# Kernel optimization log

Hardware: AMD Instinct MI355X
Metric: run time of the kernel (lower is better)

The kernel has to match this reference:

```python
import jax, jax.numpy as jnp
import numpy as np

N, CIN, T, V = 16, 16, 512, 200
K, COUT, H = 3, 64, 64


def setup_inputs() -> dict:
    key = jax.random.key(0)
    ks = jax.random.split(key, 9)
    s = 0.05
    return {
        "x": jax.random.normal(ks[0], (N, CIN, T, V), jnp.float32),
        "A": jax.random.uniform(ks[1], (K, V, V), jnp.float32) / V,
        "W_gcn": jax.random.normal(ks[2], (K * COUT, CIN), jnp.float32) * s,
        "b_gcn": jnp.zeros((K * COUT,), jnp.float32),
        "W_ih": jax.random.normal(ks[3], (4 * H, COUT), jnp.float32) * s,
        "W_hh": jax.random.normal(ks[4], (4 * H, H), jnp.float32) * s,
        "b_ih": jnp.zeros((4 * H,), jnp.float32),
        "b_hh": jnp.zeros((4 * H,), jnp.float32),
        "W_fc": jax.random.normal(ks[5], (1, H), jnp.float32) * s,
        "b_fc": jnp.zeros((1,), jnp.float32),
    }


def reference(x, A, W_gcn, b_gcn, W_ih, W_hh, b_ih, b_hh, W_fc, b_fc):
    n, c, t, v = x.shape
    k = A.shape[0]
    cout = W_gcn.shape[0] // k
    # ConvTemporalGraphical: 1x1 conv -> (n, k*cout, t, v), reshape, adjacency einsum
    y = jnp.einsum('nctv,oc->notv', x, W_gcn) + b_gcn[None, :, None, None]
    y = y.reshape(n, k, cout, t, v)
    y = jnp.einsum('nkctv,kvw->nctw', y, A)  # (n, cout, t, v)
    # mean over node dim, residual=False -> res=0
    y = jnp.mean(y, axis=3)  # (n, cout, t)
    seq = jnp.transpose(y, (2, 0, 1))  # (t, n, cout) time-major for scan

    def step(carry, xt):
        h, ccell = carry
        gates = xt @ W_ih.T + b_ih + h @ W_hh.T + b_hh  # (n, 4H)
        i, f, g, o = jnp.split(gates, 4, axis=-1)  # torch LSTM gate order
        i = jax.nn.sigmoid(i)
        f = jax.nn.sigmoid(f)
        g = jnp.tanh(g)
        o = jax.nn.sigmoid(o)
        ccell = f * ccell + i * g
        h = o * jnp.tanh(ccell)
        return (h, ccell), None

    h0 = jnp.zeros((n, W_hh.shape[1]), x.dtype)
    (h_last, _), _ = jax.lax.scan(step, (h0, h0), seq)
    out = h_last @ W_fc.T + b_fc  # (n, 1)
    return (out, A)
```

## Files before the change

kernel.cpp:

```cpp
#include <hip/hip_runtime.h>
#include <math.h>

#define N_    16
#define CIN_  16
#define T_    512
#define V_    200
#define K_    3
#define COUT_ 64
#define H_    64
#define G_    256

#define WS_A  0
#define WS_SA 640
#define WS_XA 1024
#define WS_XW (WS_XA + N_ * T_ * K_ * CIN_)

__device__ __forceinline__ float fast_sig(float x) {
    return __builtin_amdgcn_rcpf(1.f + __expf(-x));
}
__device__ __forceinline__ float fast_tanh(float x) {
    return fmaf(-2.f, __builtin_amdgcn_rcpf(1.f + __expf(2.f * x)), 1.f);
}

#define NCOPY ((K_ * V_ * V_ + 255) / 256)
__global__ __launch_bounds__(256) void prep_kernel(const float* __restrict__ A,
                                                   float* __restrict__ out,
                                                   float* __restrict__ ws) {
    int b = blockIdx.x;
    if (b < NCOPY) {
        int tid = b * 256 + threadIdx.x;
        if (tid < K_ * V_ * V_) out[16 + tid] = A[tid];
        if (tid < K_ * V_) {
            const float* row = A + (long)tid * V_;
            float s = 0.f;
            for (int w = 0; w < V_; ++w) s += row[w];
            ws[WS_A + tid] = s * (1.0f / V_);
        }
    } else {
        int k = b - NCOPY;
        const float* Ak = A + (long)k * V_ * V_;
        float s = 0.f;
        for (int i = threadIdx.x; i < V_ * V_; i += 256) s += Ak[i];
        #pragma unroll
        for (int m = 1; m < 64; m <<= 1) s += __shfl_xor(s, m);
        __shared__ float red[4];
        if ((threadIdx.x & 63) == 0) red[threadIdx.x >> 6] = s;
        __syncthreads();
        if (threadIdx.x == 0)
            ws[WS_SA + k] = (red[0] + red[1] + red[2] + red[3]) * (1.0f / V_);
    }
}

#define TT 64
#define PADV 204
__global__ __launch_bounds__(256) void xa_kernel(const float* __restrict__ x,
                                                 float* __restrict__ ws) {
    __shared__ __align__(16) float xt[TT * PADV];
    __shared__ __align__(16) float aS[K_ * V_];
    int tid = threadIdx.x;
    int b = blockIdx.x;
    int tchunk = b & 7;
    int ci = (b >> 3) & 15;
    int n = b >> 7;
    int t0 = tchunk * TT;

    for (int i = tid; i < K_ * V_; i += 256) aS[i] = ws[WS_A + i];

    const float4* xg4 =
        (const float4*)(x + ((long)(n * CIN_ + ci) * T_ + t0) * V_);
    for (int j = tid; j < TT * (V_ / 4); j += 256) {
        float4 v = xg4[j];
        int t = j / (V_ / 4), v4 = (j % (V_ / 4)) * 4;
        *(float4*)(xt + t * PADV + v4) = v;
    }
    __syncthreads();

    int t_local = tid & 63;
    int k = tid >> 6;
    if (k < K_) {
        const float* xr = xt + t_local * PADV;
        const float* ar = aS + k * V_;
        float a0 = 0.f, a1 = 0.f, a2 = 0.f, a3 = 0.f;
        #pragma unroll 5
        for (int v4 = 0; v4 < V_; v4 += 4) {
            float4 xv = *(const float4*)(xr + v4);
            float4 av = *(const float4*)(ar + v4);
            a0 = fmaf(xv.x, av.x, a0);
            a1 = fmaf(xv.y, av.y, a1);
            a2 = fmaf(xv.z, av.z, a2);
            a3 = fmaf(xv.w, av.w, a3);
        }
        float s = (a0 + a1) + (a2 + a3);
        ws[WS_XA + ((long)n * T_ + (t0 + t_local)) * (K_ * CIN_) + k * CIN_ + ci] = s;
    }
}

__global__ __launch_bounds__(256) void seqgates_kernel(
    const float* __restrict__ W_gcn, const float* __restrict__ b_gcn,
    const float* __restrict__ W_ih, const float* __restrict__ b_ih,
    const float* __restrict__ b_hh, float* __restrict__ ws) {
    int t = blockIdx.x;
    int tid = threadIdx.x;
    __shared__ float xaS[N_][K_ * CIN_];
    __shared__ __align__(16) float seqS[N_][COUT_];
    __shared__ float saS[K_];

    if (tid < K_) saS[tid] = ws[WS_SA + tid];
    #pragma unroll
    for (int r = 0; r < 3; ++r) {
        int i = tid + r * 256;
        if (i < N_ * K_ * CIN_) {
            int n = i / (K_ * CIN_), kc = i % (K_ * CIN_);
            xaS[n][kc] = ws[WS_XA + (long)(n * T_ + t) * (K_ * CIN_) + kc];
        }
    }
    __syncthreads();

    {
        int n = tid >> 4, c0 = (tid & 15) * 4;
        #pragma unroll
        for (int cc = 0; cc < 4; ++cc) {
            int c = c0 + cc;
            float s = 0.f;
            #pragma unroll
            for (int k = 0; k < K_; ++k) {
                s = fmaf(b_gcn[k * COUT_ + c], saS[k], s);
                const float* wrow = W_gcn + (long)(k * COUT_ + c) * CIN_;
                #pragma unroll
                for (int ci = 0; ci < CIN_; ++ci)
                    s = fmaf(wrow[ci], xaS[n][k * CIN_ + ci], s);
            }
            seqS[n][c] = s;
        }
    }
    __syncthreads();

    {
        int g = tid;
        float acc[N_];
        #pragma unroll
        for (int n = 0; n < N_; ++n) acc[n] = 0.f;
        const float4* wrow4 = (const float4*)(W_ih + (long)g * H_);
        #pragma unroll
        for (int c4 = 0; c4 < H_ / 4; ++c4) {
            float4 w4 = wrow4[c4];
            #pragma unroll
            for (int n = 0; n < N_; ++n) {
                float4 s4 = ((const float4*)seqS[n])[c4];
                acc[n] = fmaf(w4.x, s4.x, acc[n]);
                acc[n] = fmaf(w4.y, s4.y, acc[n]);
                acc[n] = fmaf(w4.z, s4.z, acc[n]);
                acc[n] = fmaf(w4.w, s4.w, acc[n]);
            }
        }
        float bias = b_ih[g] + b_hh[g];
        #pragma unroll
        for (int n = 0; n < N_; ++n)
            ws[WS_XW + (long)(t * N_ + n) * G_ + g] = acc[n] + bias;
    }
}

__global__ __launch_bounds__(256, 1) void lstm_kernel(
    const float* __restrict__ W_hh, const float* __restrict__ W_fc,
    const float* __restrict__ b_fc, const float* __restrict__ ws,
    float* __restrict__ out) {
    int n = blockIdx.x;
    int w = threadIdx.x >> 6;
    int lane = threadIdx.x & 63;

    const float4* wr = (const float4*)(W_hh + (long)(w * H_ + lane) * H_);
    float4 w0  = wr[0],  w1  = wr[1],  w2  = wr[2],  w3  = wr[3];
    float4 w4  = wr[4],  w5  = wr[5],  w6  = wr[6],  w7  = wr[7];
    float4 w8  = wr[8],  w9  = wr[9],  w10 = wr[10], w11 = wr[11];
    float4 w12 = wr[12], w13 = wr[13], w14 = wr[14], w15 = wr[15];

    __shared__ __align__(16) float hS[H_];
    __shared__ float gbuf[4][H_];

    if (threadIdx.x < H_) hS[threadIdx.x] = 0.f;
    float ccell = 0.f, hlast = 0.f;
    __syncthreads();

    const float* xw = ws + WS_XW + (long)n * G_ + (w * H_ + lane);
    float x0 = xw[0];
    float x1 = xw[(long)N_ * G_];

    for (int t = 0; t < T_; ++t) {
        float gate = x0;
        x0 = x1;
        if (t + 2 < T_) x1 = xw[(long)(t + 2) * N_ * G_];

        float a0 = 0.f, a1 = 0.f, a2 = 0.f, a3 = 0.f;
        const float4* h4 = (const float4*)hS;
        #define DOT4(i)                          \
            {                                    \
                float4 hv = h4[i];               \
                a0 = fmaf(w##i.x, hv.x, a0);     \
                a1 = fmaf(w##i.y, hv.y, a1);     \
                a2 = fmaf(w##i.z, hv.z, a2);     \
                a3 = fmaf(w##i.w, hv.w, a3);     \
            }
        DOT4(0)  DOT4(1)  DOT4(2)  DOT4(3)
        DOT4(4)  DOT4(5)  DOT4(6)  DOT4(7)
        DOT4(8)  DOT4(9)  DOT4(10) DOT4(11)
        DOT4(12) DOT4(13) DOT4(14) DOT4(15)
        #undef DOT4
        gate += (a0 + a1) + (a2 + a3);

        gbuf[w][lane] = gate;
        __syncthreads();
        if (w == 0) {
            float iv = fast_sig(gate);
            float fv = fast_sig(gbuf[1][lane]);
            float gv = fast_tanh(gbuf[2][lane]);
            float ov = fast_sig(gbuf[3][lane]);
            ccell = fmaf(fv, ccell, iv * gv);
            hlast = ov * fast_tanh(ccell);
            hS[lane] = hlast;
        }
        __syncthreads();
    }

    if (w == 0) {
        float p = hlast * W_fc[lane];
        #pragma unroll
        for (int m = 1; m < 64; m <<= 1) p += __shfl_xor(p, m);
        if (lane == 0) out[n] = p + b_fc[0];
    }
}

extern "C" void kernel_launch(void* const* d_in, const int* in_sizes, int n_in,
                              void* d_out, int out_size, void* d_ws, size_t ws_size,
                              hipStream_t stream) {
    const float* x     = (const float*)d_in[0];
    const float* A     = (const float*)d_in[1];
    const float* W_gcn = (const float*)d_in[2];
    const float* b_gcn = (const float*)d_in[3];
    const float* W_ih  = (const float*)d_in[4];
    const float* W_hh  = (const float*)d_in[5];
    const float* b_ih  = (const float*)d_in[6];
    const float* b_hh  = (const float*)d_in[7];
    const float* W_fc  = (const float*)d_in[8];
    const float* b_fc  = (const float*)d_in[9];
    float* out = (float*)d_out;
    float* ws  = (float*)d_ws;

    prep_kernel<<<NCOPY + K_, 256, 0, stream>>>(A, out, ws);
    xa_kernel<<<N_ * CIN_ * (T_ / TT), 256, 0, stream>>>(x, ws);
    seqgates_kernel<<<T_, 256, 0, stream>>>(W_gcn, b_gcn, W_ih, b_ih, b_hh, ws);
    lstm_kernel<<<N_, 256, 0, stream>>>(W_hh, W_fc, b_fc, ws, out);
}
```

Before: 366.6 us.

## Run LSTM recurrence for all batches in one block using split-bf16 MFMA

The LSTM recurrence now runs as a single workgroup that handles all 16 batch rows together. Each step's h·W_hh product is done with 16x16x32 bf16 MFMA instructions. Fp32 accuracy is approximated with a hi/lo bf16 split that uses three cross terms. The input-gate precompute is rewritten into a layout that matches the MFMA accumulator, h is double-buffered in LDS so each step needs only one barrier, and gate activations are computed in registers. This removes the per-step gbuf exchange and the work serialized on wave 0, at the cost of running one CU and a slight loss of precision from the bf16 split.

```diff
diff --git a/kernel.cpp b/kernel.cpp
--- a/kernel.cpp
+++ b/kernel.cpp
@@ -15,11 +15,22 @@
 #define WS_XA 1024
 #define WS_XW (WS_XA + N_ * T_ * K_ * CIN_)
 
+typedef __attribute__((ext_vector_type(8))) short short8;
+typedef __attribute__((ext_vector_type(4))) float f32x4;
+
 __device__ __forceinline__ float fast_sig(float x) {
     return __builtin_amdgcn_rcpf(1.f + __expf(-x));
 }
 __device__ __forceinline__ float fast_tanh(float x) {
     return fmaf(-2.f, __builtin_amdgcn_rcpf(1.f + __expf(2.f * x)), 1.f);
+}
+__device__ __forceinline__ unsigned short f2bf(float f) {
+    unsigned u = __float_as_uint(f);
+    u += 0x7FFFu + ((u >> 16) & 1u);
+    return (unsigned short)(u >> 16);
+}
+__device__ __forceinline__ float bf2f(unsigned short s) {
+    return __uint_as_float(((unsigned)s) << 16);
 }
 
 #define NCOPY ((K_ * V_ * V_ + 255) / 256)
@@ -154,78 +165,126 @@
             }
         }
         float bias = b_ih[g] + b_hh[g];
-        #pragma unroll
-        for (int n = 0; n < N_; ++n)
-            ws[WS_XW + (long)(t * N_ + n) * G_ + g] = acc[n] + bias;
-    }
-}
-
+        int wv = (g >> 4) & 3, ty = g >> 6, col = g & 15;
+        float4* xwf4 = (float4*)(ws + WS_XW);
+        #pragma unroll
+        for (int nb = 0; nb < 4; ++nb) {
+            float4 o4;
+            o4.x = acc[4 * nb + 0] + bias;
+            o4.y = acc[4 * nb + 1] + bias;
+            o4.z = acc[4 * nb + 2] + bias;
+            o4.w = acc[4 * nb + 3] + bias;
+            xwf4[(((long)t * 4 + wv) * 4 + ty) * 64 + nb * 16 + col] = o4;
+        }
+    }
+}
+
+#define PADC 72
 __global__ __launch_bounds__(256, 1) void lstm_kernel(
     const float* __restrict__ W_hh, const float* __restrict__ W_fc,
     const float* __restrict__ b_fc, const float* __restrict__ ws,
     float* __restrict__ out) {
-    int n = blockIdx.x;
-    int w = threadIdx.x >> 6;
-    int lane = threadIdx.x & 63;
-
-    const float4* wr = (const float4*)(W_hh + (long)(w * H_ + lane) * H_);
-    float4 w0  = wr[0],  w1  = wr[1],  w2  = wr[2],  w3  = wr[3];
-    float4 w4  = wr[4],  w5  = wr[5],  w6  = wr[6],  w7  = wr[7];
-    float4 w8  = wr[8],  w9  = wr[9],  w10 = wr[10], w11 = wr[11];
-    float4 w12 = wr[12], w13 = wr[13], w14 = wr[14], w15 = wr[15];
-
-    __shared__ __align__(16) float hS[H_];
-    __shared__ float gbuf[4][H_];
-
-    if (threadIdx.x < H_) hS[threadIdx.x] = 0.f;
-    float ccell = 0.f, hlast = 0.f;
-    __syncthreads();
-
-    const float* xw = ws + WS_XW + (long)n * G_ + (w * H_ + lane);
-    float x0 = xw[0];
-    float x1 = xw[(long)N_ * G_];
+    int tid = threadIdx.x;
+    int w = tid >> 6;
+    int l = tid & 63;
+    int lg = l >> 4, ll = l & 15;
+
+    short8 bhi[4][2], blo[4][2];
+    #pragma unroll
+    for (int ty = 0; ty < 4; ++ty) {
+        #pragma unroll
+        for (int ks = 0; ks < 2; ++ks) {
+            const float* wp = W_hh + (long)(ty * 64 + 16 * w + ll) * H_ + ks * 32 + 8 * lg;
+            short8 hi, lo;
+            #pragma unroll
+            for (int i = 0; i < 8; ++i) {
+                float wv = wp[i];
+                unsigned short hb = f2bf(wv);
+                hi[i] = (short)hb;
+                lo[i] = (short)f2bf(wv - bf2f(hb));
+            }
+            bhi[ty][ks] = hi;
+            blo[ty][ks] = lo;
+        }
+    }
+    #pragma unroll
+    for (int ty = 0; ty < 4; ++ty)
+        #pragma unroll
+        for (int ks = 0; ks < 2; ++ks)
+            asm volatile("" : "+v"(bhi[ty][ks]), "+v"(blo[ty][ks]));
+
+    __shared__ __align__(16) unsigned short Ahi[2][16][PADC];
+    __shared__ __align__(16) unsigned short Alo[2][16][PADC];
+    __shared__ __align__(16) float hf[16][64];
+
+    for (int i = tid; i < 16 * PADC; i += 256) {
+        (&Ahi[0][0][0])[i] = 0;
+        (&Alo[0][0][0])[i] = 0;
+    }
+
+    const f32x4* xwf = (const f32x4*)(ws + WS_XW);
+    f32x4 xcur[4], xnxt[4];
+    #pragma unroll
+    for (int ty = 0; ty < 4; ++ty) xcur[ty] = xwf[((0 * 4 + w) * 4 + ty) * 64 + l];
+    #pragma unroll
+    for (int ty = 0; ty < 4; ++ty) xnxt[ty] = xwf[((1 * 4 + w) * 4 + ty) * 64 + l];
+
+    float cst[4] = {0.f, 0.f, 0.f, 0.f};
+    float hout[4] = {0.f, 0.f, 0.f, 0.f};
+    __syncthreads();
 
     for (int t = 0; t < T_; ++t) {
-        float gate = x0;
-        x0 = x1;
-        if (t + 2 < T_) x1 = xw[(long)(t + 2) * N_ * G_];
-
-        float a0 = 0.f, a1 = 0.f, a2 = 0.f, a3 = 0.f;
-        const float4* h4 = (const float4*)hS;
-        #define DOT4(i)                          \
-            {                                    \
-                float4 hv = h4[i];               \
-                a0 = fmaf(w##i.x, hv.x, a0);     \
-                a1 = fmaf(w##i.y, hv.y, a1);     \
-                a2 = fmaf(w##i.z, hv.z, a2);     \
-                a3 = fmaf(w##i.w, hv.w, a3);     \
-            }
-        DOT4(0)  DOT4(1)  DOT4(2)  DOT4(3)
-        DOT4(4)  DOT4(5)  DOT4(6)  DOT4(7)
-        DOT4(8)  DOT4(9)  DOT4(10) DOT4(11)
-        DOT4(12) DOT4(13) DOT4(14) DOT4(15)
-        #undef DOT4
-        gate += (a0 + a1) + (a2 + a3);
-
-        gbuf[w][lane] = gate;
+        int p = t & 1;
+        short8 ahi0 = *(const short8*)&Ahi[p][ll][0 * 32 + 8 * lg];
+        short8 ahi1 = *(const short8*)&Ahi[p][ll][1 * 32 + 8 * lg];
+        short8 alo0 = *(const short8*)&Alo[p][ll][0 * 32 + 8 * lg];
+        short8 alo1 = *(const short8*)&Alo[p][ll][1 * 32 + 8 * lg];
+
+        f32x4 acc[4];
+        #pragma unroll
+        for (int ty = 0; ty < 4; ++ty) {
+            f32x4 a = xcur[ty];
+            a = __builtin_amdgcn_mfma_f32_16x16x32_bf16(ahi0, bhi[ty][0], a, 0, 0, 0);
+            a = __builtin_amdgcn_mfma_f32_16x16x32_bf16(ahi1, bhi[ty][1], a, 0, 0, 0);
+            a = __builtin_amdgcn_mfma_f32_16x16x32_bf16(ahi0, blo[ty][0], a, 0, 0, 0);
+            a = __builtin_amdgcn_mfma_f32_16x16x32_bf16(ahi1, blo[ty][1], a, 0, 0, 0);
+            a = __builtin_amdgcn_mfma_f32_16x16x32_bf16(alo0, bhi[ty][0], a, 0, 0, 0);
+            a = __builtin_amdgcn_mfma_f32_16x16x32_bf16(alo1, bhi[ty][1], a, 0, 0, 0);
+            acc[ty] = a;
+        }
+        #pragma unroll
+        for (int ty = 0; ty < 4; ++ty) xcur[ty] = xnxt[ty];
+        if (t + 2 < T_) {
+            #pragma unroll
+            for (int ty = 0; ty < 4; ++ty)
+                xnxt[ty] = xwf[(((long)(t + 2) * 4 + w) * 4 + ty) * 64 + l];
+        }
+        #pragma unroll
+        for (int r = 0; r < 4; ++r) {
+            float iv = fast_sig(acc[0][r]);
+            float fv = fast_sig(acc[1][r]);
+            float gv = fast_tanh(acc[2][r]);
+            float ov = fast_sig(acc[3][r]);
+            cst[r] = fmaf(fv, cst[r], iv * gv);
+            hout[r] = ov * fast_tanh(cst[r]);
+        }
+        #pragma unroll
+        for (int r = 0; r < 4; ++r) {
+            int n = 4 * lg + r, j = 16 * w + ll;
+            unsigned short hb = f2bf(hout[r]);
+            Ahi[p ^ 1][n][j] = hb;
+            Alo[p ^ 1][n][j] = f2bf(hout[r] - bf2f(hb));
+        }
         __syncthreads();
-        if (w == 0) {
-            float iv = fast_sig(gate);
-            float fv = fast_sig(gbuf[1][lane]);
-            float gv = fast_tanh(gbuf[2][lane]);
-            float ov = fast_sig(gbuf[3][lane]);
-            ccell = fmaf(fv, ccell, iv * gv);
-            hlast = ov * fast_tanh(ccell);
-            hS[lane] = hlast;
-        }
-        __syncthreads();
-    }
-
-    if (w == 0) {
-        float p = hlast * W_fc[lane];
-        #pragma unroll
-        for (int m = 1; m < 64; m <<= 1) p += __shfl_xor(p, m);
-        if (lane == 0) out[n] = p + b_fc[0];
+    }
+
+    #pragma unroll
+    for (int r = 0; r < 4; ++r) hf[4 * lg + r][16 * w + ll] = hout[r];
+    __syncthreads();
+    if (tid < N_) {
+        float s = 0.f;
+        for (int j = 0; j < H_; ++j) s = fmaf(hf[tid][j], W_fc[j], s);
+        out[tid] = s + b_fc[0];
     }
 }
 
@@ -248,5 +307,5 @@
     prep_kernel<<<NCOPY + K_, 256, 0, stream>>>(A, out, ws);
     xa_kernel<<<N_ * CIN_ * (T_ / TT), 256, 0, stream>>>(x, ws);
     seqgates_kernel<<<T_, 256, 0, stream>>>(W_gcn, b_gcn, W_ih, b_ih, b_hh, ws);
-    lstm_kernel<<<N_, 256, 0, stream>>>(W_hh, W_fc, b_fc, ws, out);
-}
+    lstm_kernel<<<1, 256, 0, stream>>>(W_hh, W_fc, b_fc, ws, out);
+}
```

Result: slower. 498.9 us (+36.1%).

## Regroup LSTM gates per wave, exchange via shuffles, double-buffer hidden state

Applied to the files above, without the earlier changes.

A new prep block writes a permuted copy of W_hh to the workspace. Each wave then owns the i, f, g and o gate rows for the same 16 hidden units. Every lane applies its own activation (tanh is expressed through a scaled sigmoid), and the gate values are gathered with cross-lane shuffles instead of an LDS gate buffer. With the hidden state double-buffered in shared memory, each recurrent step needs one barrier instead of two, which shortens the serial per-step latency. The cost is that weights are read through a workspace pointer inside the loop, which relies on the compiler hoisting them into registers, plus an extra prep copy.

```diff
diff --git a/kernel.cpp b/kernel.cpp
--- a/kernel.cpp
+++ b/kernel.cpp
@@ -14,6 +14,7 @@
 #define WS_SA 640
 #define WS_XA 1024
 #define WS_XW (WS_XA + N_ * T_ * K_ * CIN_)
+#define WS_WP (WS_XW + T_ * N_ * G_)
 
 __device__ __forceinline__ float fast_sig(float x) {
     return __builtin_amdgcn_rcpf(1.f + __expf(-x));
@@ -24,6 +25,7 @@
 
 #define NCOPY ((K_ * V_ * V_ + 255) / 256)
 __global__ __launch_bounds__(256) void prep_kernel(const float* __restrict__ A,
+                                                   const float* __restrict__ W_hh,
                                                    float* __restrict__ out,
                                                    float* __restrict__ ws) {
     int b = blockIdx.x;
@@ -36,7 +38,7 @@
             for (int w = 0; w < V_; ++w) s += row[w];
             ws[WS_A + tid] = s * (1.0f / V_);
         }
-    } else {
+    } else if (b < NCOPY + K_) {
         int k = b - NCOPY;
         const float* Ak = A + (long)k * V_ * V_;
         float s = 0.f;
@@ -48,6 +50,12 @@
         __syncthreads();
         if (threadIdx.x == 0)
             ws[WS_SA + k] = (red[0] + red[1] + red[2] + red[3]) * (1.0f / V_);
+    } else {
+        int tid = threadIdx.x;
+        int w = tid >> 6, ty = (tid >> 4) & 3, jj = tid & 15;
+        const float* src = W_hh + (long)(ty * 64 + 16 * w + jj) * H_;
+        float* dst = ws + WS_WP + (long)tid * H_;
+        for (int c = 0; c < H_; ++c) dst[c] = src[c];
     }
 }
 
@@ -161,71 +169,66 @@
 }
 
 __global__ __launch_bounds__(256, 1) void lstm_kernel(
-    const float* __restrict__ W_hh, const float* __restrict__ W_fc,
-    const float* __restrict__ b_fc, const float* __restrict__ ws,
-    float* __restrict__ out) {
+    const float* __restrict__ W_fc, const float* __restrict__ b_fc,
+    const float* __restrict__ ws, float* __restrict__ out) {
     int n = blockIdx.x;
-    int w = threadIdx.x >> 6;
-    int lane = threadIdx.x & 63;
-
-    const float4* wr = (const float4*)(W_hh + (long)(w * H_ + lane) * H_);
-    float4 w0  = wr[0],  w1  = wr[1],  w2  = wr[2],  w3  = wr[3];
-    float4 w4  = wr[4],  w5  = wr[5],  w6  = wr[6],  w7  = wr[7];
-    float4 w8  = wr[8],  w9  = wr[9],  w10 = wr[10], w11 = wr[11];
-    float4 w12 = wr[12], w13 = wr[13], w14 = wr[14], w15 = wr[15];
-
-    __shared__ __align__(16) float hS[H_];
-    __shared__ float gbuf[4][H_];
-
-    if (threadIdx.x < H_) hS[threadIdx.x] = 0.f;
-    float ccell = 0.f, hlast = 0.f;
-    __syncthreads();
-
-    const float* xw = ws + WS_XW + (long)n * G_ + (w * H_ + lane);
+    int tid = threadIdx.x;
+    int w = tid >> 6;
+    int lane = tid & 63;
+    int ty = lane >> 4;
+    int jj = lane & 15;
+
+    const float4* wp4 = (const float4*)(ws + WS_WP + (long)tid * H_);
+
+    float s_act = (ty == 2) ? 2.f : 1.f;
+    float m_act = (ty == 2) ? 2.f : 1.f;
+    float b_act = (ty == 2) ? -1.f : 0.f;
+
+    __shared__ __align__(16) float hS[2][H_];
+    if (tid < H_) hS[0][tid] = 0.f;
+    float ccell = 0.f;
+    __syncthreads();
+
+    const float* xw = ws + WS_XW + (long)n * G_ + (ty * 64 + 16 * w + jj);
     float x0 = xw[0];
     float x1 = xw[(long)N_ * G_];
 
     for (int t = 0; t < T_; ++t) {
+        int p = t & 1;
         float gate = x0;
         x0 = x1;
         if (t + 2 < T_) x1 = xw[(long)(t + 2) * N_ * G_];
 
         float a0 = 0.f, a1 = 0.f, a2 = 0.f, a3 = 0.f;
-        const float4* h4 = (const float4*)hS;
-        #define DOT4(i)                          \
-            {                                    \
-                float4 hv = h4[i];               \
-                a0 = fmaf(w##i.x, hv.x, a0);     \
-                a1 = fmaf(w##i.y, hv.y, a1);     \
-                a2 = fmaf(w##i.z, hv.z, a2);     \
-                a3 = fmaf(w##i.w, hv.w, a3);     \
-            }
-        DOT4(0)  DOT4(1)  DOT4(2)  DOT4(3)
-        DOT4(4)  DOT4(5)  DOT4(6)  DOT4(7)
-        DOT4(8)  DOT4(9)  DOT4(10) DOT4(11)
-        DOT4(12) DOT4(13) DOT4(14) DOT4(15)
-        #undef DOT4
+        const float4* h4 = (const float4*)hS[p];
+        #pragma unroll
+        for (int i = 0; i < 16; ++i) {
+            float4 wv = wp4[i];
+            float4 hv = h4[i];
+            a0 = fmaf(wv.x, hv.x, a0);
+            a1 = fmaf(wv.y, hv.y, a1);
+            a2 = fmaf(wv.z, hv.z, a2);
+            a3 = fmaf(wv.w, hv.w, a3);
+        }
         gate += (a0 + a1) + (a2 + a3);
 
-        gbuf[w][lane] = gate;
+        float act = fmaf(m_act, fast_sig(s_act * gate), b_act);
+        float fv = __shfl(act, 16 + jj);
+        float gv = __shfl(act, 32 + jj);
+        float ov = __shfl(act, 48 + jj);
+        if (ty == 0) {
+            ccell = fmaf(fv, ccell, act * gv);
+            float h = ov * fast_tanh(ccell);
+            hS[p ^ 1][16 * w + jj] = h;
+        }
         __syncthreads();
-        if (w == 0) {
-            float iv = fast_sig(gate);
-            float fv = fast_sig(gbuf[1][lane]);
-            float gv = fast_tanh(gbuf[2][lane]);
-            float ov = fast_sig(gbuf[3][lane]);
-            ccell = fmaf(fv, ccell, iv * gv);
-            hlast = ov * fast_tanh(ccell);
-            hS[lane] = hlast;
-        }
-        __syncthreads();
-    }
-
-    if (w == 0) {
-        float p = hlast * W_fc[lane];
-        #pragma unroll
-        for (int m = 1; m < 64; m <<= 1) p += __shfl_xor(p, m);
-        if (lane == 0) out[n] = p + b_fc[0];
+    }
+
+    if (tid < H_) {
+        float pv = hS[0][tid] * W_fc[tid];
+        #pragma unroll
+        for (int m = 1; m < 64; m <<= 1) pv += __shfl_xor(pv, m);
+        if (tid == 0) out[n] = pv + b_fc[0];
     }
 }
 
@@ -245,8 +248,8 @@
     float* out = (float*)d_out;
     float* ws  = (float*)d_ws;
 
-    prep_kernel<<<NCOPY + K_, 256, 0, stream>>>(A, out, ws);
+    prep_kernel<<<NCOPY + K_ + 1, 256, 0, stream>>>(A, W_hh, out, ws);
     xa_kernel<<<N_ * CIN_ * (T_ / TT), 256, 0, stream>>>(x, ws);
     seqgates_kernel<<<T_, 256, 0, stream>>>(W_gcn, b_gcn, W_ih, b_ih, b_hh, ws);
-    lstm_kernel<<<N_, 256, 0, stream>>>(W_hh, W_fc, b_fc, ws, out);
-}
+    lstm_kernel<<<N_, 256, 0, stream>>>(W_fc, b_fc, ws, out);
+}
```

New measurement: 359.2 us. 1.02x faster.
